# Performance work log

Hardware: AMD Instinct MI355X
Metric: run time of the kernel (lower is better)

The kernel has to match this reference:

```python
import jax, jax.numpy as jnp
import numpy as np

# WFLW 98-point curve decomposition: (start, end) landmark index ranges (end exclusive)
CURVES = [(0, 33), (33, 42), (42, 51), (51, 60), (60, 68), (68, 76), (76, 88), (88, 98)]
SIGMA_W2 = [15.0] * len(CURVES)  # get_sigmaV2(...)/4, constant per curve
N_PT = 98
LEFT_EYE, RIGHT_EYE = 60, 72  # eye-corner indices for the 98-point branch


def curve_loss(p, g, sigma_w2):
    # p, g: [B, n, 2] landmarks of one facial curve
    c_p = (p[:, :-1] + p[:, 1:]) * 0.5   # segment centers, [B, n-1, 2]
    tau_p = p[:, 1:] - p[:, :-1]          # segment tangents, [B, n-1, 2]
    c_g = (g[:, :-1] + g[:, 1:]) * 0.5
    tau_g = g[:, 1:] - g[:, :-1]
    c = jnp.concatenate([c_p, c_g], axis=1)        # [B, M, 2], M = 2*(n-1)
    tau = jnp.concatenate([tau_p, -tau_g], axis=1)  # [B, M, 2]
    # pairwise RBF kernel on segment centers: exp(-||c_i - c_j||^2 / sigma)
    d2 = jnp.sum((c[:, :, None, :] - c[:, None, :, :]) ** 2, axis=-1)  # [B, M, M]
    weight = jnp.exp(-d2 / sigma_w2)
    dot = jnp.einsum('bid,bjd->bij', tau, tau)  # pairwise tangent dot products
    return jnp.sum(weight * dot, axis=(1, 2))   # [B]


def reference(pred, gt):
    batch = pred.shape[0]
    pl = pred.reshape(batch, -1, 2)  # [B, 98, 2]
    gl = gt.reshape(batch, -1, 2)
    mean_error = jnp.mean(jnp.linalg.norm(pl - gl, axis=-1), axis=-1)  # [B]
    eye_dist = jnp.linalg.norm(gl[:, LEFT_EYE] - gl[:, RIGHT_EYE], axis=-1)  # [B]
    landmark_error = jnp.mean(mean_error / eye_dist)
    curve_error = jnp.zeros((batch,), dtype=pred.dtype)
    for (a, b), s2 in zip(CURVES, SIGMA_W2):
        curve_error = curve_error + curve_loss(pl[:, a:b], gl[:, a:b], s2)
    curve_error = jnp.mean(curve_error / (N_PT * eye_dist))
    return 0.8 * landmark_error + 0.2 * curve_error


def setup_inputs() -> dict:
    key = jax.random.key(0)
    k1, k2 = jax.random.split(key)
    pred = jax.random.normal(k1, (16384, 196), dtype=jnp.float32)
    gt = jax.random.normal(k2, (16384, 196), dtype=jnp.float32)
    return {"pred": pred, "gt": gt}
```

## Files before the change

### kernel.cpp

```cpp
#include <hip/hip_runtime.h>
#include <math.h>

static constexpr int NPT = 98;
static constexpr float CSCALE_HALF = 0.155064240f;

#if __has_builtin(__builtin_amdgcn_exp2f)
#define EXP2F(x) __builtin_amdgcn_exp2f(x)
#else
#define EXP2F(x) exp2f(x)
#endif
#if __has_builtin(__builtin_amdgcn_sqrtf)
#define SQRTF(x) __builtin_amdgcn_sqrtf(x)
#else
#define SQRTF(x) sqrtf(x)
#endif

typedef float v2f __attribute__((ext_vector_type(2)));
typedef float v4a __attribute__((ext_vector_type(4)));
typedef float v4fu __attribute__((ext_vector_type(4), aligned(8)));
typedef _Float16 h2 __attribute__((ext_vector_type(2)));
typedef _Float16 h4 __attribute__((ext_vector_type(4)));

#if __has_builtin(__builtin_amdgcn_fdot2)
#define FDOT2(a, b, c) __builtin_amdgcn_fdot2((a), (b), (c), false)
#else
#define FDOT2(a, b, c) fmaf((float)(a).x, (float)(b).x, fmaf((float)(a).y, (float)(b).y, (c)))
#endif

#if __has_builtin(__builtin_amdgcn_cvt_pkrtz)
#define PKRTZ(x, y) __builtin_bit_cast(h2, __builtin_amdgcn_cvt_pkrtz((x), (y)))
#else
static __device__ __forceinline__ h2 PKRTZ(float x, float y) {
    h2 r; r.x = (_Float16)x; r.y = (_Float16)y; return r;
}
#endif


struct SLut { unsigned v[192]; };
static constexpr SLut make_slut() {
    SLut L{};
    constexpr int A[8]  = {0, 33, 42, 51, 60, 68, 76, 88};
    constexpr int NS[8] = {32, 8, 8, 8, 7, 7, 11, 9};
    constexpr int BB[8] = {0, 96, 118, 140, 162, 182, 202, 230};
    int s = 0;
    for (int c = 0; c < 8; ++c) {
        int dupn = (c == 0) ? 32 : 6;
        for (int rel = 0; rel < 2 * NS[c]; ++rel, ++s) {
            bool isg = rel >= NS[c];
            int a = A[c] + (isg ? rel - NS[c] : rel);
            int dst = BB[c] + rel;
            int dup = (rel < dupn) ? (BB[c] + 2 * NS[c] + rel) : 255;
            L.v[s] = (unsigned)a | (isg ? 0x80u : 0u)
                   | ((unsigned)dst << 8) | ((unsigned)dup << 16);
        }
    }
    for (; s < 192; ++s) L.v[s] = 0u | (254u << 8) | (255u << 16);
    return L;
}
__constant__ SLut cSLUT = make_slut();

struct BLut { unsigned v[64]; };
static constexpr BLut make_blut() {
    BLut L{};
    constexpr int lo[8]   = {0, 8, 16, 24, 31, 38, 49, 58};
    constexpr int bs[8]   = {96, 118, 140, 162, 182, 202, 230, 202};
    constexpr int hh[8]   = {8, 8, 8, 7, 7, 11, 9, 11};
    constexpr int ta[8]   = {4, 4, 4, 3, 3, 5, 4, 0};
    constexpr int tb[8]   = {3, 3, 3, 3, 3, 5, 4, 0};
    constexpr int mmv[8]  = {1, 1, 1, 1, 1, 1, 1, 0};
    for (int g = 0; g < 8; ++g) {
        int hi = (g < 7) ? lo[g + 1] : 64;
        for (int l = lo[g]; l < hi; ++l) {
            int off = bs[g] + ((g < 7) ? (l - lo[g]) : 0);
            L.v[l] = (unsigned)off | ((unsigned)hh[g] << 8)
                   | ((unsigned)ta[g] << 12) | ((unsigned)tb[g] << 15)
                   | ((unsigned)mmv[g] << 18);
        }
    }
    return L;
}
__constant__ BLut cBLUT = make_blut();

__device__ __forceinline__ float wdt(h4 si, h4 sj) {
    h2 dc = si.xy - sj.xy;
    float d2 = FDOT2(dc, dc, 0.0f);
    float dt = FDOT2(si.zw, sj.zw, 0.0f);
    return EXP2F(-d2) * dt;
}

__global__ __launch_bounds__(256, 4)
void lddmm_main(const float* __restrict__ pred, const float* __restrict__ gt,
                float* __restrict__ ws) {
    __shared__ h4 sh[4][256];
    const int wave = threadIdx.x >> 6;
    const int lane = threadIdx.x & 63;
    __builtin_assume(lane < 64);
    const int b = blockIdx.x * 4 + wave;

    const float* pf = pred + (size_t)b * (2 * NPT);
    const float* gf = gt + (size_t)b * (2 * NPT);
    const v2f* g2 = (const v2f*)gf;
    h4* sw = sh[wave];

    v2f e0 = g2[60];
    v2f e1 = g2[72];

    float diag = 0.0f;
    float accS = 0.0f;
    float accA = 0.0f;
    float accB = 0.0f;
    float dsum = 0.0f;

    #pragma unroll
    for (int pass = 0; pass < 3; ++pass) {
        int s = lane + 64 * pass;
        if (s < 180) {
            unsigned e = cSLUT.v[s];
            int a = e & 0x7f;
            bool isg = (e & 0x80u) != 0;
            int dst = (int)((e >> 8) & 0xffu);
            int dup = (int)((e >> 16) & 0xffu);
            const float* src = isg ? gf : pf;
            v4fu q = *(const v4fu*)(src + 2 * a);
            v2f c = (q.xy + q.zw) * CSCALE_HALF;
            v2f tau = q.zw - q.xy;
            if (isg) tau = -tau;
            diag = fmaf(tau.x, tau.x, diag);
            diag = fmaf(tau.y, tau.y, diag);
            h2 ch = PKRTZ(c.x, c.y);
            h2 th = PKRTZ(tau.x, tau.y);
            h4 v; v.x = ch.x; v.y = ch.y; v.z = th.x; v.w = th.y;
            sw[dst] = v;
            if (dup != 255) sw[dup] = v;
        }
    }

    if (lane < 49) {
        v4a p4 = *(const v4a*)(pf + 4 * lane);
        v4a g4 = *(const v4a*)(gf + 4 * lane);
        v2f d0 = p4.xy - g4.xy;
        v2f d1 = p4.zw - g4.zw;
        dsum = SQRTF(d0.x * d0.x + d0.y * d0.y)
             + SQRTF(d1.x * d1.x + d1.y * d1.y);
    }

    asm volatile("s_waitcnt lgkmcnt(0)" ::: "memory");

    {
        h4 sjA = sw[lane];
        h4 sjB = sw[lane + 32];
        #pragma unroll 8
        for (int t = 1; t <= 15; ++t) {
            h4 r = sw[lane + t];
            accA += wdt(r, sjA);
            accB += wdt(r, sjB);
        }
        { h4 r = sw[lane + 16]; accA += wdt(r, sjA); }
        accS += wdt(sjA, sjB);
    }

    {
        unsigned e = cBLUT.v[lane];
        const h4* sp = sw + (e & 0xffu);
        int h = (int)((e >> 8) & 0xfu);
        int TA = (int)((e >> 12) & 7u);
        int TB = (int)((e >> 15) & 7u);
        float mm = (e & (1u << 18)) ? 1.0f : 0.0f;
        h4 sjA = sp[0];
        h4 sjB = sp[h];
        accA = fmaf(mm, wdt(sjA, sjB), accA);
        #pragma unroll
        for (int t = 1; t <= 5; ++t) {
            h4 u1 = sp[t];
            h4 u2 = sp[h + t];
            float mA = (t <= TA) ? 1.0f : 0.0f;
            float mB = (t <= TB) ? 1.0f : 0.0f;
            accA = fmaf(mA, wdt(u1, sjA) + wdt(u2, sjB), accA);
            accB = fmaf(mB, wdt(u1, sjB) + wdt(u2, sjA), accB);
        }
    }

    float v = 0.8f * dsum + 0.2f * (fmaf(2.0f, accA + accB, diag + accS));
    #pragma unroll
    for (int off = 32; off >= 1; off >>= 1) v += __shfl_xor(v, off, 64);

    if (lane == 0) {
        v2f de = e0 - e1;
        float eye = SQRTF(de.x * de.x + de.y * de.y);
        ws[b] = v / ((float)NPT * eye);
    }
}

__global__ __launch_bounds__(1024)
void lddmm_reduce(const float* __restrict__ ws, float* __restrict__ out,
                  int n4, float invbatch) {
    __shared__ float sm[1024];
    const int t = threadIdx.x;
    const float4* w4 = (const float4*)ws;
    float s = 0.0f;
    for (int i = t; i < n4; i += 1024) {
        float4 v = w4[i];
        s += (v.x + v.y) + (v.z + v.w);
    }
    sm[t] = s;
    __syncthreads();
    for (int off = 512; off >= 1; off >>= 1) {
        if (t < off) sm[t] += sm[t + off];
        __syncthreads();
    }
    if (t == 0) out[0] = sm[0] * invbatch;
}

extern "C" void kernel_launch(void* const* d_in, const int* in_sizes, int n_in,
                              void* d_out, int out_size, void* d_ws, size_t ws_size,
                              hipStream_t stream) {
    const float* pred = (const float*)d_in[0];
    const float* gt = (const float*)d_in[1];
    float* out = (float*)d_out;
    float* ws = (float*)d_ws;
    const int batch = in_sizes[0] / (2 * NPT);

    lddmm_main<<<batch / 4, 256, 0, stream>>>(pred, gt, ws);
    lddmm_reduce<<<1, 1024, 0, stream>>>(ws, out, batch / 4, 1.0f / (float)batch);
}
```

Measured before the change: 26.52 us.

## Split each batch element across two waves with shared partial reduction

Each batch element is now handled by two wavefronts instead of one, so a 256-thread block covers two elements and the grid doubles. The segment-staging loads, landmark distance terms and pairwise kernel loops are divided between the two waves, and their partial sums are combined through shared memory after a block barrier. The aim is to shorten each wave's serial chain of LDS reads and exp evaluations and to expose more parallelism. The cost is twice as many waves, two __syncthreads barriers in place of a wave-local waitcnt, and some duplicated setup work.

```diff
diff --git a/kernel.cpp b/kernel.cpp
--- a/kernel.cpp
+++ b/kernel.cpp
@@ -91,19 +91,22 @@
 __global__ __launch_bounds__(256, 4)
 void lddmm_main(const float* __restrict__ pred, const float* __restrict__ gt,
                 float* __restrict__ ws) {
-    __shared__ h4 sh[4][256];
-    const int wave = threadIdx.x >> 6;
-    const int lane = threadIdx.x & 63;
+    __shared__ h4 sh[2][256];
+    __shared__ float part[2][2];
+    const int tid = threadIdx.x;
+    const int wave = tid >> 6;
+    const int lane = tid & 63;
     __builtin_assume(lane < 64);
-    const int b = blockIdx.x * 4 + wave;
+    const int eidx = wave >> 1;
+    const int wv = wave & 1;
+    const int b = blockIdx.x * 2 + eidx;
 
     const float* pf = pred + (size_t)b * (2 * NPT);
     const float* gf = gt + (size_t)b * (2 * NPT);
-    const v2f* g2 = (const v2f*)gf;
-    h4* sw = sh[wave];
-
-    v2f e0 = g2[60];
-    v2f e1 = g2[72];
+    h4* sw = sh[eidx];
+
+    v2f e0 = ((const v2f*)gf)[60];
+    v2f e1 = ((const v2f*)gf)[72];
 
     float diag = 0.0f;
     float accS = 0.0f;
@@ -111,10 +114,29 @@
     float accB = 0.0f;
     float dsum = 0.0f;
 
-    #pragma unroll
-    for (int pass = 0; pass < 3; ++pass) {
-        int s = lane + 64 * pass;
-        if (s < 180) {
+    {
+        int s = lane + 64 * wv;
+        unsigned e = cSLUT.v[s];
+        int a = e & 0x7f;
+        bool isg = (e & 0x80u) != 0;
+        int dst = (int)((e >> 8) & 0xffu);
+        int dup = (int)((e >> 16) & 0xffu);
+        const float* src = isg ? gf : pf;
+        v4fu q = *(const v4fu*)(src + 2 * a);
+        v2f c = (q.xy + q.zw) * CSCALE_HALF;
+        v2f tau = q.zw - q.xy;
+        if (isg) tau = -tau;
+        diag = fmaf(tau.x, tau.x, diag);
+        diag = fmaf(tau.y, tau.y, diag);
+        h2 ch = PKRTZ(c.x, c.y);
+        h2 th = PKRTZ(tau.x, tau.y);
+        h4 v; v.x = ch.x; v.y = ch.y; v.z = th.x; v.w = th.y;
+        sw[dst] = v;
+        if (dup != 255) sw[dup] = v;
+    }
+    {
+        int s = 128 + 26 * wv + lane;
+        if (lane < 26) {
             unsigned e = cSLUT.v[s];
             int a = e & 0x7f;
             bool isg = (e & 0x80u) != 0;
@@ -135,28 +157,41 @@
         }
     }
 
-    if (lane < 49) {
-        v4a p4 = *(const v4a*)(pf + 4 * lane);
-        v4a g4 = *(const v4a*)(gf + 4 * lane);
-        v2f d0 = p4.xy - g4.xy;
-        v2f d1 = p4.zw - g4.zw;
-        dsum = SQRTF(d0.x * d0.x + d0.y * d0.y)
-             + SQRTF(d1.x * d1.x + d1.y * d1.y);
-    }
-
-    asm volatile("s_waitcnt lgkmcnt(0)" ::: "memory");
+    {
+        bool act = wv ? (lane < 24) : (lane < 25);
+        if (act) {
+            int off = wv ? (100 + 4 * lane) : (4 * lane);
+            v4a p4 = *(const v4a*)(pf + off);
+            v4a g4 = *(const v4a*)(gf + off);
+            v2f d0 = p4.xy - g4.xy;
+            v2f d1 = p4.zw - g4.zw;
+            dsum = SQRTF(d0.x * d0.x + d0.y * d0.y)
+                 + SQRTF(d1.x * d1.x + d1.y * d1.y);
+        }
+    }
+
+    __syncthreads();
 
     {
         h4 sjA = sw[lane];
         h4 sjB = sw[lane + 32];
-        #pragma unroll 8
-        for (int t = 1; t <= 15; ++t) {
-            h4 r = sw[lane + t];
-            accA += wdt(r, sjA);
-            accB += wdt(r, sjB);
-        }
-        { h4 r = sw[lane + 16]; accA += wdt(r, sjA); }
-        accS += wdt(sjA, sjB);
+        if (wv == 0) {
+            #pragma unroll
+            for (int t = 1; t <= 8; ++t) {
+                h4 r = sw[lane + t];
+                accA += wdt(r, sjA);
+                accB += wdt(r, sjB);
+            }
+        } else {
+            #pragma unroll
+            for (int t = 9; t <= 15; ++t) {
+                h4 r = sw[lane + t];
+                accA += wdt(r, sjA);
+                accB += wdt(r, sjB);
+            }
+            { h4 r = sw[lane + 16]; accA += wdt(r, sjA); }
+            accS += wdt(sjA, sjB);
+        }
     }
 
     {
@@ -165,29 +200,44 @@
         int h = (int)((e >> 8) & 0xfu);
         int TA = (int)((e >> 12) & 7u);
         int TB = (int)((e >> 15) & 7u);
-        float mm = (e & (1u << 18)) ? 1.0f : 0.0f;
         h4 sjA = sp[0];
         h4 sjB = sp[h];
-        accA = fmaf(mm, wdt(sjA, sjB), accA);
-        #pragma unroll
-        for (int t = 1; t <= 5; ++t) {
-            h4 u1 = sp[t];
-            h4 u2 = sp[h + t];
-            float mA = (t <= TA) ? 1.0f : 0.0f;
-            float mB = (t <= TB) ? 1.0f : 0.0f;
-            accA = fmaf(mA, wdt(u1, sjA) + wdt(u2, sjB), accA);
-            accB = fmaf(mB, wdt(u1, sjB) + wdt(u2, sjA), accB);
+        if (wv == 0) {
+            #pragma unroll
+            for (int t = 1; t <= 3; ++t) {
+                h4 u1 = sp[t];
+                h4 u2 = sp[h + t];
+                float mA = (t <= TA) ? 1.0f : 0.0f;
+                float mB = (t <= TB) ? 1.0f : 0.0f;
+                accA = fmaf(mA, wdt(u1, sjA) + wdt(u2, sjB), accA);
+                accB = fmaf(mB, wdt(u1, sjB) + wdt(u2, sjA), accB);
+            }
+        } else {
+            float mm = (e & (1u << 18)) ? 1.0f : 0.0f;
+            accA = fmaf(mm, wdt(sjA, sjB), accA);
+            #pragma unroll
+            for (int t = 4; t <= 5; ++t) {
+                h4 u1 = sp[t];
+                h4 u2 = sp[h + t];
+                float mA = (t <= TA) ? 1.0f : 0.0f;
+                float mB = (t <= TB) ? 1.0f : 0.0f;
+                accA = fmaf(mA, wdt(u1, sjA) + wdt(u2, sjB), accA);
+                accB = fmaf(mB, wdt(u1, sjB) + wdt(u2, sjA), accB);
+            }
         }
     }
 
     float v = 0.8f * dsum + 0.2f * (fmaf(2.0f, accA + accB, diag + accS));
     #pragma unroll
     for (int off = 32; off >= 1; off >>= 1) v += __shfl_xor(v, off, 64);
-
-    if (lane == 0) {
+    if (lane == 0) part[eidx][wv] = v;
+    __syncthreads();
+
+    if ((tid & 127) == 0) {
+        float tot = part[eidx][0] + part[eidx][1];
         v2f de = e0 - e1;
         float eye = SQRTF(de.x * de.x + de.y * de.y);
-        ws[b] = v / ((float)NPT * eye);
+        ws[b] = tot / ((float)NPT * eye);
     }
 }
 
@@ -220,6 +270,7 @@
     float* ws = (float*)d_ws;
     const int batch = in_sizes[0] / (2 * NPT);
 
-    lddmm_main<<<batch / 4, 256, 0, stream>>>(pred, gt, ws);
+    const int nblk = batch / 2;
+    lddmm_main<<<nblk, 256, 0, stream>>>(pred, gt, ws);
     lddmm_reduce<<<1, 1024, 0, stream>>>(ws, out, batch / 4, 1.0f / (float)batch);
 }
```

After: 28.94 us. 1.09x slower.
